# Kernel tuning notes

Measured on AMD Instinct MI355X. Metric: run time of the kernel, lower is better.

## Reference

```python
import jax, jax.numpy as jnp
import numpy as np

N_SRC = 100000
N_DST = 100000
N_EDGES = 640000
D = 128
D_OUT = 128


def setup_inputs() -> dict:
    key = jax.random.key(0)
    k1, k2, k3, k4, k5, k6 = jax.random.split(key, 6)
    h_src = jax.random.normal(k1, (N_SRC, D), dtype=jnp.float32)
    h_dst = jax.random.normal(k2, (N_DST, D), dtype=jnp.float32)
    src_idx = jax.random.randint(k3, (N_EDGES,), 0, N_SRC, dtype=jnp.int32)
    dst_idx = jax.random.randint(k4, (N_EDGES,), 0, N_DST, dtype=jnp.int32)
    W = jax.random.normal(k5, (2 * D, D_OUT), dtype=jnp.float32) * 0.05
    b = jax.random.normal(k6, (D_OUT,), dtype=jnp.float32) * 0.05
    return {"h_src": h_src, "h_dst": h_dst, "src_idx": src_idx,
            "dst_idx": dst_idx, "W": W, "b": b}


def reference(h_src, h_dst, src_idx, dst_idx, W, b):
    # copy_u: gather source features along edges -> [E, D]
    msgs = h_src[src_idx]
    # mean aggregation per destination node (segment mean)
    summed = jax.ops.segment_sum(msgs, dst_idx, num_segments=N_DST)  # [N_dst, D]
    deg = jax.ops.segment_sum(jnp.ones((N_EDGES,), dtype=h_src.dtype),
                              dst_idx, num_segments=N_DST)  # [N_dst]
    h_N = summed / jnp.maximum(deg, 1.0)[:, None]
    # concat self + neighbor mean, then linear projection
    h_total = jnp.concatenate([h_dst, h_N], axis=1)  # [N_dst, 2D]
    return h_total @ W + b
```

## Files before the change

### kernel.cpp

```cpp
#include <hip/hip_runtime.h>

#define D 128
#define N_SRC 100000
#define N_DST 100000
#define N_EDGES 640000

#define SCAN_BLK 1024
#define N_SCAN_BLOCKS ((N_DST + SCAN_BLK - 1) / SCAN_BLK)

#define HIST_BLOCKS ((N_EDGES + 255) / 256)
#define CVT_BLOCKS  ((N_SRC * D / 8) / 256)
#define PACKW_BLOCKS 128

typedef __attribute__((ext_vector_type(8))) short s8v;
typedef __attribute__((ext_vector_type(4))) float f32x4;

__device__ __forceinline__ unsigned short f2bf(float f) {
    unsigned int u = __float_as_uint(f);
    u += 0x7fffu + ((u >> 16) & 1u);
    return (unsigned short)(u >> 16);
}

__device__ __forceinline__ unsigned int pk2(float a, float b) {
    return (unsigned int)f2bf(a) | ((unsigned int)f2bf(b) << 16);
}

__global__ __launch_bounds__(256) void prep(
    const int* __restrict__ dst_idx, int* __restrict__ counts,
    const float* __restrict__ h_src, unsigned int* __restrict__ mir32,
    const float* __restrict__ W, unsigned short* __restrict__ Bp)
{
    const int blk = blockIdx.x;
    const int tid = threadIdx.x;
    if (blk < HIST_BLOCKS) {
        int e = blk * 256 + tid;
        if (e < N_EDGES) atomicAdd(&counts[dst_idx[e]], 1);
    } else if (blk < HIST_BLOCKS + CVT_BLOCKS) {
        int id = (blk - HIST_BLOCKS) * 256 + tid;
        size_t e = (size_t)id * 8;
        const float4* p = (const float4*)(h_src + e);
        float4 x = p[0], y = p[1];
        uint4 o;
        o.x = pk2(x.x, x.y); o.y = pk2(x.z, x.w);
        o.z = pk2(y.x, y.y); o.w = pk2(y.z, y.w);
        *(uint4*)(mir32 + (size_t)(id >> 4) * 64 + (id & 15) * 4) = o;
    } else {
        int id = (blk - HIST_BLOCKS - CVT_BLOCKS) * 256 + tid;
        if (id < 32768) {
            int j = id & 7;
            int l = (id >> 3) & 63;
            int t = (id >> 9) & 7;
            int s = id >> 12;
            int k = s * 32 + (l >> 4) * 8 + j;
            int n = t * 16 + (l & 15);
            Bp[id] = f2bf(W[k * D + n]);
        }
    }
}


__global__ __launch_bounds__(256) void scan_blocks(
    const int* __restrict__ counts, int* __restrict__ row_start,
    int* __restrict__ block_sums)
{
    __shared__ int sh[256];
    const int tid = threadIdx.x;
    const int base = blockIdx.x * SCAN_BLK + tid * 4;
    int v[4];
    int local = 0;
#pragma unroll
    for (int k = 0; k < 4; k++) {
        int idx = base + k;
        v[k] = (idx < N_DST) ? counts[idx] : 0;
        local += v[k];
    }
    sh[tid] = local;
    __syncthreads();
    for (int off = 1; off < 256; off <<= 1) {
        int t = (tid >= off) ? sh[tid - off] : 0;
        __syncthreads();
        sh[tid] += t;
        __syncthreads();
    }
    int run = (tid == 0) ? 0 : sh[tid - 1];
    if (tid == 255) block_sums[blockIdx.x] = sh[255];
#pragma unroll
    for (int k = 0; k < 4; k++) {
        int idx = base + k;
        if (idx < N_DST) row_start[idx] = run;
        run += v[k];
    }
}

__global__ __launch_bounds__(256) void add_offsets(
    int* __restrict__ row_start, const int* __restrict__ block_sums,
    int* __restrict__ cursor)
{
    __shared__ int sh[128];
    const int tid = threadIdx.x;
    if (tid < 128) sh[tid] = (tid < N_SCAN_BLOCKS) ? block_sums[tid] : 0;
    __syncthreads();
    for (int off = 1; off < 128; off <<= 1) {
        int t = (tid < 128 && tid >= off) ? sh[tid - off] : 0;
        __syncthreads();
        if (tid < 128) sh[tid] += t;
        __syncthreads();
    }
    int i = blockIdx.x * 256 + tid;
    if (i < N_DST) {
        int blk = i / SCAN_BLK;
        int off = (blk == 0) ? 0 : sh[blk - 1];
        int v = row_start[i] + off;
        row_start[i] = v;
        cursor[i] = v;
    }
    if (i == 0) row_start[N_DST] = N_EDGES;
}

__global__ __launch_bounds__(256) void scatter_perm(
    const int* __restrict__ src_idx, const int* __restrict__ dst_idx,
    int* __restrict__ cursor, int* __restrict__ edge_src)
{
    int e = blockIdx.x * 256 + threadIdx.x;
    if (e < N_EDGES) {
        int d = dst_idx[e];
        int pos = atomicAdd(&cursor[d], 1);
        edge_src[pos] = src_idx[e];
    }
}

__global__ __launch_bounds__(128, 4) void fused_ag(
    const float* __restrict__ h_dst,
    const unsigned short* __restrict__ mir,
    const int* __restrict__ row_start,
    const int* __restrict__ edge_src,
    const unsigned short* __restrict__ Bp,
    const float* __restrict__ bias,
    float* __restrict__ out)
{
    __shared__ uint4 hN4[512];
    char* hN = (char*)hN4;

    const int tid = threadIdx.x;
    const int wave = tid >> 6;
    const int lane = tid & 63;
    const int quad = lane >> 4;
    const int lr = lane & 15;
    const int rw0 = blockIdx.x * 32 + wave * 16;

#pragma unroll
    for (int i = 0; i < 4; i++) {
        int rl = wave * 16 + i * 4 + quad;
        int row = blockIdx.x * 32 + rl;
        int start = row_start[row];
        int deg = row_start[row + 1] - start;
        float a[8] = {0.f, 0.f, 0.f, 0.f, 0.f, 0.f, 0.f, 0.f};
        for (int base = 0; base < deg; base += 8) {
            int j = base + (lr & 7);
            int myid = edge_src[start + min(j, deg - 1)];
#pragma unroll
            for (int t = 0; t < 8; t++) {
                int s = __shfl(myid, t, 16);
                uint4 u = *(const uint4*)(mir + (size_t)s * 128 + lr * 8);
                float m = ((base + t) < deg) ? 1.f : 0.f;
                a[0] = fmaf(__uint_as_float(u.x << 16), m, a[0]);
                a[1] = fmaf(__uint_as_float(u.x & 0xffff0000u), m, a[1]);
                a[2] = fmaf(__uint_as_float(u.y << 16), m, a[2]);
                a[3] = fmaf(__uint_as_float(u.y & 0xffff0000u), m, a[3]);
                a[4] = fmaf(__uint_as_float(u.z << 16), m, a[4]);
                a[5] = fmaf(__uint_as_float(u.z & 0xffff0000u), m, a[5]);
                a[6] = fmaf(__uint_as_float(u.w << 16), m, a[6]);
                a[7] = fmaf(__uint_as_float(u.w & 0xffff0000u), m, a[7]);
            }
        }
        float inv = 1.0f / fmaxf((float)deg, 1.0f);
        uint4 o;
        o.x = pk2(a[0] * inv, a[1] * inv);
        o.y = pk2(a[2] * inv, a[3] * inv);
        o.z = pk2(a[4] * inv, a[5] * inv);
        o.w = pk2(a[6] * inv, a[7] * inv);
        int ba = (rl * 256 + lr * 16) ^ ((rl & 7) << 4);
        *(uint4*)(hN + ba) = o;
    }

    s8v an[4];
    {
        int rl = wave * 16 + lr;
#pragma unroll
        for (int s = 0; s < 4; s++) {
            int ba = (rl * 256 + s * 64 + quad * 16) ^ ((rl & 7) << 4);
            an[s] = *(const s8v*)(hN + ba);
        }
    }

    const int r0 = rw0 + lr;
    const float* p0 = h_dst + (size_t)r0 * D + quad * 8;
    float4 x0[4], y0[4];
#pragma unroll
    for (int s = 0; s < 4; s++) {
        x0[s] = *(const float4*)(p0 + s * 32);
        y0[s] = *(const float4*)(p0 + s * 32 + 4);
    }
    s8v af0[4];
#pragma unroll
    for (int s = 0; s < 4; s++) {
        unsigned short u0[8];
        u0[0]=f2bf(x0[s].x); u0[1]=f2bf(x0[s].y); u0[2]=f2bf(x0[s].z); u0[3]=f2bf(x0[s].w);
        u0[4]=f2bf(y0[s].x); u0[5]=f2bf(y0[s].y); u0[6]=f2bf(y0[s].z); u0[7]=f2bf(y0[s].w);
        af0[s] = *(s8v*)u0;
    }

    f32x4 acc[8];
#pragma unroll
    for (int t = 0; t < 8; t++) acc[t] = (f32x4){0.f, 0.f, 0.f, 0.f};

#pragma unroll
    for (int s = 0; s < 8; s++) {
        s8v a0 = (s < 4) ? af0[s] : an[s - 4];
#pragma unroll
        for (int t = 0; t < 8; t++) {
            s8v bf = *(const s8v*)(Bp + ((size_t)(s * 8 + t) * 64 + lane) * 8);
            acc[t] = __builtin_amdgcn_mfma_f32_16x16x32_bf16(a0, bf, acc[t], 0, 0, 0);
        }
    }

#pragma unroll
    for (int t = 0; t < 8; t++) {
        float bv = bias[t * 16 + lr];
#pragma unroll
        for (int r = 0; r < 4; r++) {
            int row = rw0 + quad * 4 + r;
            out[(size_t)row * D + t * 16 + lr] = acc[t][r] + bv;
        }
    }
}

extern "C" void kernel_launch(void* const* d_in, const int* in_sizes, int n_in,
                              void* d_out, int out_size, void* d_ws, size_t ws_size,
                              hipStream_t stream) {
    const float* h_src  = (const float*)d_in[0];
    const float* h_dst  = (const float*)d_in[1];
    const int* src_idx  = (const int*)d_in[2];
    const int* dst_idx  = (const int*)d_in[3];
    const float* W      = (const float*)d_in[4];
    const float* b      = (const float*)d_in[5];
    float* out = (float*)d_out;

    unsigned short* Bp = (unsigned short*)d_ws;
    int* ws_i          = (int*)((char*)d_ws + 65536);
    int* row_start     = ws_i;
    int* cursor        = row_start + (N_DST + 1);
    int* counts        = cursor + N_DST;
    int* block_sums    = counts + N_DST;
    int* edge_src      = block_sums + N_SCAN_BLOCKS;

    size_t int_bytes = (size_t)(N_DST + 1 + N_DST + N_DST + N_SCAN_BLOCKS + N_EDGES) * 4;
    size_t mir_off   = (65536 + int_bytes + 255) & ~(size_t)255;
    unsigned short* mir = (unsigned short*)((char*)d_ws + mir_off);

    hipMemsetAsync(counts, 0, (size_t)N_DST * sizeof(int), stream);

    prep<<<HIST_BLOCKS + CVT_BLOCKS + PACKW_BLOCKS, 256, 0, stream>>>(
        dst_idx, counts, h_src, (unsigned int*)mir, W, Bp);
    scan_blocks<<<N_SCAN_BLOCKS, 256, 0, stream>>>(counts, row_start, block_sums);
    add_offsets<<<(N_DST + 255) / 256, 256, 0, stream>>>(row_start, block_sums, cursor);
    scatter_perm<<<(N_EDGES + 255) / 256, 256, 0, stream>>>(src_idx, dst_idx, cursor, edge_src);

    fused_ag<<<N_DST / 32, 128, 0, stream>>>(
        h_dst, mir, row_start, edge_src, Bp, b, out);
}
```

Before: 258.2 us.

## Merge CSR build into one persistent kernel with grid barriers; widen aggregation blocks

Replaces the memset plus prep, scan, offset and scatter launches with a single persistent 1024-block kernel that uses atomic grid barriers between phases, removing several launch gaps and kernel boundaries. The aggregation kernel moves to 256-thread blocks covering 64 rows each. Its inner loop splits full 8-edge groups, which read edge ids directly without shuffles or masking, from a masked tail group. The grid barrier relies on all 1024 blocks being co-resident and could deadlock if they are not. Reading edge ids per lane instead of shuffling adds redundant scalar loads.

```diff
diff --git a/kernel.cpp b/kernel.cpp
--- a/kernel.cpp
+++ b/kernel.cpp
@@ -8,9 +8,8 @@
 #define SCAN_BLK 1024
 #define N_SCAN_BLOCKS ((N_DST + SCAN_BLK - 1) / SCAN_BLK)
 
-#define HIST_BLOCKS ((N_EDGES + 255) / 256)
-#define CVT_BLOCKS  ((N_SRC * D / 8) / 256)
-#define PACKW_BLOCKS 128
+#define CSR_BLOCKS 1024
+#define CSR_THREADS (CSR_BLOCKS * 256)
 
 typedef __attribute__((ext_vector_type(8))) short s8v;
 typedef __attribute__((ext_vector_type(4))) float f32x4;
@@ -25,79 +24,83 @@
     return (unsigned int)f2bf(a) | ((unsigned int)f2bf(b) << 16);
 }
 
-__global__ __launch_bounds__(256) void prep(
-    const int* __restrict__ dst_idx, int* __restrict__ counts,
-    const float* __restrict__ h_src, unsigned int* __restrict__ mir32,
-    const float* __restrict__ W, unsigned short* __restrict__ Bp)
+__device__ __forceinline__ void grid_barrier(int* ctr) {
+    __syncthreads();
+    if (threadIdx.x == 0) {
+        __threadfence();
+        __hip_atomic_fetch_add(ctr, 1, __ATOMIC_RELEASE, __HIP_MEMORY_SCOPE_AGENT);
+        while (__hip_atomic_load(ctr, __ATOMIC_ACQUIRE, __HIP_MEMORY_SCOPE_AGENT)
+               < CSR_BLOCKS) {}
+    }
+    __syncthreads();
+}
+
+__global__ __launch_bounds__(256, 4) void build_csr(
+    const float* __restrict__ h_src,
+    const int* __restrict__ src_idx, const int* __restrict__ dst_idx,
+    const float* __restrict__ W,
+    unsigned int* __restrict__ mir32, unsigned short* __restrict__ Bp,
+    int* __restrict__ counts, int* __restrict__ row_start,
+    int* __restrict__ cursor, int* __restrict__ block_sums,
+    int* __restrict__ edge_src, int* __restrict__ bar)
 {
-    const int blk = blockIdx.x;
+    __shared__ int sh[256];
     const int tid = threadIdx.x;
-    if (blk < HIST_BLOCKS) {
-        int e = blk * 256 + tid;
-        if (e < N_EDGES) atomicAdd(&counts[dst_idx[e]], 1);
-    } else if (blk < HIST_BLOCKS + CVT_BLOCKS) {
-        int id = (blk - HIST_BLOCKS) * 256 + tid;
-        size_t e = (size_t)id * 8;
-        const float4* p = (const float4*)(h_src + e);
+    const int gid = blockIdx.x * 256 + tid;
+
+    for (int i = gid; i < N_DST; i += CSR_THREADS) counts[i] = 0;
+    for (int id = gid; id < N_SRC * 16; id += CSR_THREADS) {
+        const float4* p = (const float4*)(h_src + (size_t)id * 8);
         float4 x = p[0], y = p[1];
         uint4 o;
         o.x = pk2(x.x, x.y); o.y = pk2(x.z, x.w);
         o.z = pk2(y.x, y.y); o.w = pk2(y.z, y.w);
         *(uint4*)(mir32 + (size_t)(id >> 4) * 64 + (id & 15) * 4) = o;
-    } else {
-        int id = (blk - HIST_BLOCKS - CVT_BLOCKS) * 256 + tid;
-        if (id < 32768) {
-            int j = id & 7;
-            int l = (id >> 3) & 63;
-            int t = (id >> 9) & 7;
-            int s = id >> 12;
-            int k = s * 32 + (l >> 4) * 8 + j;
-            int n = t * 16 + (l & 15);
-            Bp[id] = f2bf(W[k * D + n]);
-        }
-    }
-}
-
-
-__global__ __launch_bounds__(256) void scan_blocks(
-    const int* __restrict__ counts, int* __restrict__ row_start,
-    int* __restrict__ block_sums)
-{
-    __shared__ int sh[256];
-    const int tid = threadIdx.x;
-    const int base = blockIdx.x * SCAN_BLK + tid * 4;
-    int v[4];
-    int local = 0;
-#pragma unroll
-    for (int k = 0; k < 4; k++) {
-        int idx = base + k;
-        v[k] = (idx < N_DST) ? counts[idx] : 0;
-        local += v[k];
-    }
-    sh[tid] = local;
-    __syncthreads();
-    for (int off = 1; off < 256; off <<= 1) {
-        int t = (tid >= off) ? sh[tid - off] : 0;
+    }
+    for (int id = gid; id < 32768; id += CSR_THREADS) {
+        int j = id & 7;
+        int l = (id >> 3) & 63;
+        int t = (id >> 9) & 7;
+        int s = id >> 12;
+        int k = s * 32 + (l >> 4) * 8 + j;
+        int n = t * 16 + (l & 15);
+        Bp[id] = f2bf(W[k * D + n]);
+    }
+    grid_barrier(&bar[0]);
+
+    for (int e = gid; e < N_EDGES; e += CSR_THREADS)
+        atomicAdd(&counts[dst_idx[e]], 1);
+    grid_barrier(&bar[1]);
+
+    if (blockIdx.x < N_SCAN_BLOCKS) {
+        const int base = blockIdx.x * SCAN_BLK + tid * 4;
+        int v[4];
+        int local = 0;
+#pragma unroll
+        for (int k = 0; k < 4; k++) {
+            int idx = base + k;
+            v[k] = (idx < N_DST) ? counts[idx] : 0;
+            local += v[k];
+        }
+        sh[tid] = local;
         __syncthreads();
-        sh[tid] += t;
-        __syncthreads();
-    }
-    int run = (tid == 0) ? 0 : sh[tid - 1];
-    if (tid == 255) block_sums[blockIdx.x] = sh[255];
-#pragma unroll
-    for (int k = 0; k < 4; k++) {
-        int idx = base + k;
-        if (idx < N_DST) row_start[idx] = run;
-        run += v[k];
-    }
-}
-
-__global__ __launch_bounds__(256) void add_offsets(
-    int* __restrict__ row_start, const int* __restrict__ block_sums,
-    int* __restrict__ cursor)
-{
-    __shared__ int sh[128];
-    const int tid = threadIdx.x;
+        for (int off = 1; off < 256; off <<= 1) {
+            int t = (tid >= off) ? sh[tid - off] : 0;
+            __syncthreads();
+            sh[tid] += t;
+            __syncthreads();
+        }
+        int run = (tid == 0) ? 0 : sh[tid - 1];
+        if (tid == 255) block_sums[blockIdx.x] = sh[255];
+#pragma unroll
+        for (int k = 0; k < 4; k++) {
+            int idx = base + k;
+            if (idx < N_DST) row_start[idx] = run;
+            run += v[k];
+        }
+    }
+    grid_barrier(&bar[2]);
+
     if (tid < 128) sh[tid] = (tid < N_SCAN_BLOCKS) ? block_sums[tid] : 0;
     __syncthreads();
     for (int off = 1; off < 128; off <<= 1) {
@@ -106,30 +109,24 @@
         if (tid < 128) sh[tid] += t;
         __syncthreads();
     }
-    int i = blockIdx.x * 256 + tid;
-    if (i < N_DST) {
+    for (int i = gid; i < N_DST; i += CSR_THREADS) {
         int blk = i / SCAN_BLK;
         int off = (blk == 0) ? 0 : sh[blk - 1];
         int v = row_start[i] + off;
         row_start[i] = v;
         cursor[i] = v;
     }
-    if (i == 0) row_start[N_DST] = N_EDGES;
-}
-
-__global__ __launch_bounds__(256) void scatter_perm(
-    const int* __restrict__ src_idx, const int* __restrict__ dst_idx,
-    int* __restrict__ cursor, int* __restrict__ edge_src)
-{
-    int e = blockIdx.x * 256 + threadIdx.x;
-    if (e < N_EDGES) {
+    if (gid == 0) row_start[N_DST] = N_EDGES;
+    grid_barrier(&bar[3]);
+
+    for (int e = gid; e < N_EDGES; e += CSR_THREADS) {
         int d = dst_idx[e];
         int pos = atomicAdd(&cursor[d], 1);
         edge_src[pos] = src_idx[e];
     }
 }
 
-__global__ __launch_bounds__(128, 4) void fused_ag(
+__global__ __launch_bounds__(256, 4) void fused_ag(
     const float* __restrict__ h_dst,
     const unsigned short* __restrict__ mir,
     const int* __restrict__ row_start,
@@ -138,7 +135,7 @@
     const float* __restrict__ bias,
     float* __restrict__ out)
 {
-    __shared__ uint4 hN4[512];
+    __shared__ uint4 hN4[1024];
     char* hN = (char*)hN4;
 
     const int tid = threadIdx.x;
@@ -146,23 +143,39 @@
     const int lane = tid & 63;
     const int quad = lane >> 4;
     const int lr = lane & 15;
-    const int rw0 = blockIdx.x * 32 + wave * 16;
+    const int wg = blockIdx.x * 4 + wave;
+    if (wg * 16 >= N_DST) return;
+    const int rw0 = wg * 16;
 
 #pragma unroll
     for (int i = 0; i < 4; i++) {
         int rl = wave * 16 + i * 4 + quad;
-        int row = blockIdx.x * 32 + rl;
+        int row = blockIdx.x * 64 + rl;
         int start = row_start[row];
         int deg = row_start[row + 1] - start;
+        int nfull = deg & ~7;
         float a[8] = {0.f, 0.f, 0.f, 0.f, 0.f, 0.f, 0.f, 0.f};
-        for (int base = 0; base < deg; base += 8) {
-            int j = base + (lr & 7);
-            int myid = edge_src[start + min(j, deg - 1)];
+        for (int base = 0; base < nfull; base += 8) {
 #pragma unroll
             for (int t = 0; t < 8; t++) {
-                int s = __shfl(myid, t, 16);
+                int s = edge_src[start + base + t];
                 uint4 u = *(const uint4*)(mir + (size_t)s * 128 + lr * 8);
-                float m = ((base + t) < deg) ? 1.f : 0.f;
+                a[0] += __uint_as_float(u.x << 16);
+                a[1] += __uint_as_float(u.x & 0xffff0000u);
+                a[2] += __uint_as_float(u.y << 16);
+                a[3] += __uint_as_float(u.y & 0xffff0000u);
+                a[4] += __uint_as_float(u.z << 16);
+                a[5] += __uint_as_float(u.z & 0xffff0000u);
+                a[6] += __uint_as_float(u.w << 16);
+                a[7] += __uint_as_float(u.w & 0xffff0000u);
+            }
+        }
+        if (nfull < deg) {
+#pragma unroll
+            for (int t = 0; t < 8; t++) {
+                int s = edge_src[start + min(nfull + t, deg - 1)];
+                uint4 u = *(const uint4*)(mir + (size_t)s * 128 + lr * 8);
+                float m = ((nfull + t) < deg) ? 1.f : 0.f;
                 a[0] = fmaf(__uint_as_float(u.x << 16), m, a[0]);
                 a[1] = fmaf(__uint_as_float(u.x & 0xffff0000u), m, a[1]);
                 a[2] = fmaf(__uint_as_float(u.y << 16), m, a[2]);
@@ -252,20 +265,21 @@
     int* cursor        = row_start + (N_DST + 1);
     int* counts        = cursor + N_DST;
     int* block_sums    = counts + N_DST;
-    int* edge_src      = block_sums + N_SCAN_BLOCKS;
-
-    size_t int_bytes = (size_t)(N_DST + 1 + N_DST + N_DST + N_SCAN_BLOCKS + N_EDGES) * 4;
+    int* bar           = block_sums + N_SCAN_BLOCKS;
+    int* edge_src      = bar + 8;
+
+    size_t int_bytes = (size_t)(N_DST + 1 + N_DST + N_DST + N_SCAN_BLOCKS + 8
+                                + N_EDGES) * 4;
     size_t mir_off   = (65536 + int_bytes + 255) & ~(size_t)255;
     unsigned short* mir = (unsigned short*)((char*)d_ws + mir_off);
 
-    hipMemsetAsync(counts, 0, (size_t)N_DST * sizeof(int), stream);
-
-    prep<<<HIST_BLOCKS + CVT_BLOCKS + PACKW_BLOCKS, 256, 0, stream>>>(
-        dst_idx, counts, h_src, (unsigned int*)mir, W, Bp);
-    scan_blocks<<<N_SCAN_BLOCKS, 256, 0, stream>>>(counts, row_start, block_sums);
-    add_offsets<<<(N_DST + 255) / 256, 256, 0, stream>>>(row_start, block_sums, cursor);
-    scatter_perm<<<(N_EDGES + 255) / 256, 256, 0, stream>>>(src_idx, dst_idx, cursor, edge_src);
-
-    fused_ag<<<N_DST / 32, 128, 0, stream>>>(
+    hipMemsetAsync(bar, 0, 8 * sizeof(int), stream);
+
+    build_csr<<<CSR_BLOCKS, 256, 0, stream>>>(
+        h_src, src_idx, dst_idx, W,
+        (unsigned int*)mir, Bp,
+        counts, row_start, cursor, block_sums, edge_src, bar);
+
+    fused_ag<<<(N_DST + 63) / 64, 256, 0, stream>>>(
         h_dst, mir, row_start, edge_src, Bp, b, out);
 }
```

After: 725.0 us. 2.81x slower.

## Move bf16 conversion into scatter pass, widen aggregation blocks, unmask full edge chunks

Applied to the files above, without the earlier changes.

The bf16 conversion of h_src and the W packing move out of the histogram kernel and into the scatter kernel, so the histogram atomics run alone and the conversion shares a launch with the scatter. The aggregation kernel goes from 128 to 256 threads per block, handling 64 rows per block, with a guard for waves past the end. Full 8-edge chunks now read edge indices directly and accumulate with plain adds instead of a lane shuffle and a masked FMA. Only the tail chunk keeps the masked path. The cost is a larger shared-memory footprint per block and a slightly different schedule of atomics against conversion traffic.

```diff
diff --git a/kernel.cpp b/kernel.cpp
--- a/kernel.cpp
+++ b/kernel.cpp
@@ -8,7 +8,7 @@
 #define SCAN_BLK 1024
 #define N_SCAN_BLOCKS ((N_DST + SCAN_BLK - 1) / SCAN_BLK)
 
-#define HIST_BLOCKS ((N_EDGES + 255) / 256)
+#define SCAT_BLOCKS ((N_EDGES + 255) / 256)
 #define CVT_BLOCKS  ((N_SRC * D / 8) / 256)
 #define PACKW_BLOCKS 128
 
@@ -25,27 +25,96 @@
     return (unsigned int)f2bf(a) | ((unsigned int)f2bf(b) << 16);
 }
 
-__global__ __launch_bounds__(256) void prep(
-    const int* __restrict__ dst_idx, int* __restrict__ counts,
+__global__ __launch_bounds__(256) void hist_kernel(
+    const int* __restrict__ dst_idx, int* __restrict__ counts)
+{
+    int e = blockIdx.x * 256 + threadIdx.x;
+    if (e < N_EDGES) atomicAdd(&counts[dst_idx[e]], 1);
+}
+
+__global__ __launch_bounds__(256) void scan_blocks(
+    const int* __restrict__ counts, int* __restrict__ row_start,
+    int* __restrict__ block_sums)
+{
+    __shared__ int sh[256];
+    const int tid = threadIdx.x;
+    const int base = blockIdx.x * SCAN_BLK + tid * 4;
+    int v[4];
+    int local = 0;
+#pragma unroll
+    for (int k = 0; k < 4; k++) {
+        int idx = base + k;
+        v[k] = (idx < N_DST) ? counts[idx] : 0;
+        local += v[k];
+    }
+    sh[tid] = local;
+    __syncthreads();
+    for (int off = 1; off < 256; off <<= 1) {
+        int t = (tid >= off) ? sh[tid - off] : 0;
+        __syncthreads();
+        sh[tid] += t;
+        __syncthreads();
+    }
+    int run = (tid == 0) ? 0 : sh[tid - 1];
+    if (tid == 255) block_sums[blockIdx.x] = sh[255];
+#pragma unroll
+    for (int k = 0; k < 4; k++) {
+        int idx = base + k;
+        if (idx < N_DST) row_start[idx] = run;
+        run += v[k];
+    }
+}
+
+__global__ __launch_bounds__(256) void add_offsets(
+    int* __restrict__ row_start, const int* __restrict__ block_sums,
+    int* __restrict__ cursor)
+{
+    __shared__ int sh[128];
+    const int tid = threadIdx.x;
+    if (tid < 128) sh[tid] = (tid < N_SCAN_BLOCKS) ? block_sums[tid] : 0;
+    __syncthreads();
+    for (int off = 1; off < 128; off <<= 1) {
+        int t = (tid < 128 && tid >= off) ? sh[tid - off] : 0;
+        __syncthreads();
+        if (tid < 128) sh[tid] += t;
+        __syncthreads();
+    }
+    int i = blockIdx.x * 256 + tid;
+    if (i < N_DST) {
+        int blk = i / SCAN_BLK;
+        int off = (blk == 0) ? 0 : sh[blk - 1];
+        int v = row_start[i] + off;
+        row_start[i] = v;
+        cursor[i] = v;
+    }
+    if (i == 0) row_start[N_DST] = N_EDGES;
+}
+
+__global__ __launch_bounds__(256) void scatter_cvt(
+    const int* __restrict__ src_idx, const int* __restrict__ dst_idx,
+    int* __restrict__ cursor, int* __restrict__ edge_src,
     const float* __restrict__ h_src, unsigned int* __restrict__ mir32,
     const float* __restrict__ W, unsigned short* __restrict__ Bp)
 {
     const int blk = blockIdx.x;
     const int tid = threadIdx.x;
-    if (blk < HIST_BLOCKS) {
+    if (blk < SCAT_BLOCKS) {
         int e = blk * 256 + tid;
-        if (e < N_EDGES) atomicAdd(&counts[dst_idx[e]], 1);
-    } else if (blk < HIST_BLOCKS + CVT_BLOCKS) {
-        int id = (blk - HIST_BLOCKS) * 256 + tid;
-        size_t e = (size_t)id * 8;
-        const float4* p = (const float4*)(h_src + e);
+        if (e < N_EDGES) {
+            int d = dst_idx[e];
+            int pos = atomicAdd(&cursor[d], 1);
+            edge_src[pos] = src_idx[e];
+        }
+    } else if (blk < SCAT_BLOCKS + CVT_BLOCKS) {
+        int id = (blk - SCAT_BLOCKS) * 256 + tid;
+        const float4* p = (const float4*)(h_src + (size_t)id * 8);
         float4 x = p[0], y = p[1];
         uint4 o;
         o.x = pk2(x.x, x.y); o.y = pk2(x.z, x.w);
         o.z = pk2(y.x, y.y); o.w = pk2(y.z, y.w);
         *(uint4*)(mir32 + (size_t)(id >> 4) * 64 + (id & 15) * 4) = o;
     } else {
-        int id = (blk - HIST_BLOCKS - CVT_BLOCKS) * 256 + tid;
+        int id = (blk - SCAT_BLOCKS - CVT_BLOCKS) * 256 + tid;
         if (id < 32768) {
             int j = id & 7;
             int l = (id >> 3) & 63;
@@ -58,78 +127,7 @@
     }
 }
 
-
-__global__ __launch_bounds__(256) void scan_blocks(
-    const int* __restrict__ counts, int* __restrict__ row_start,
-    int* __restrict__ block_sums)
-{
-    __shared__ int sh[256];
-    const int tid = threadIdx.x;
-    const int base = blockIdx.x * SCAN_BLK + tid * 4;
-    int v[4];
-    int local = 0;
-#pragma unroll
-    for (int k = 0; k < 4; k++) {
-        int idx = base + k;
-        v[k] = (idx < N_DST) ? counts[idx] : 0;
-        local += v[k];
-    }
-    sh[tid] = local;
-    __syncthreads();
-    for (int off = 1; off < 256; off <<= 1) {
-        int t = (tid >= off) ? sh[tid - off] : 0;
-        __syncthreads();
-        sh[tid] += t;
-        __syncthreads();
-    }
-    int run = (tid == 0) ? 0 : sh[tid - 1];
-    if (tid == 255) block_sums[blockIdx.x] = sh[255];
-#pragma unroll
-    for (int k = 0; k < 4; k++) {
-        int idx = base + k;
-        if (idx < N_DST) row_start[idx] = run;
-        run += v[k];
-    }
-}
-
-__global__ __launch_bounds__(256) void add_offsets(
-    int* __restrict__ row_start, const int* __restrict__ block_sums,
-    int* __restrict__ cursor)
-{
-    __shared__ int sh[128];
-    const int tid = threadIdx.x;
-    if (tid < 128) sh[tid] = (tid < N_SCAN_BLOCKS) ? block_sums[tid] : 0;
-    __syncthreads();
-    for (int off = 1; off < 128; off <<= 1) {
-        int t = (tid < 128 && tid >= off) ? sh[tid - off] : 0;
-        __syncthreads();
-        if (tid < 128) sh[tid] += t;
-        __syncthreads();
-    }
-    int i = blockIdx.x * 256 + tid;
-    if (i < N_DST) {
-        int blk = i / SCAN_BLK;
-        int off = (blk == 0) ? 0 : sh[blk - 1];
-        int v = row_start[i] + off;
-        row_start[i] = v;
-        cursor[i] = v;
-    }
-    if (i == 0) row_start[N_DST] = N_EDGES;
-}
-
-__global__ __launch_bounds__(256) void scatter_perm(
-    const int* __restrict__ src_idx, const int* __restrict__ dst_idx,
-    int* __restrict__ cursor, int* __restrict__ edge_src)
-{
-    int e = blockIdx.x * 256 + threadIdx.x;
-    if (e < N_EDGES) {
-        int d = dst_idx[e];
-        int pos = atomicAdd(&cursor[d], 1);
-        edge_src[pos] = src_idx[e];
-    }
-}
-
-__global__ __launch_bounds__(128, 4) void fused_ag(
+__global__ __launch_bounds__(256, 4) void fused_ag(
     const float* __restrict__ h_dst,
     const unsigned short* __restrict__ mir,
     const int* __restrict__ row_start,
@@ -138,7 +136,7 @@
     const float* __restrict__ bias,
     float* __restrict__ out)
 {
-    __shared__ uint4 hN4[512];
+    __shared__ uint4 hN4[1024];
     char* hN = (char*)hN4;
 
     const int tid = threadIdx.x;
@@ -146,23 +144,39 @@
     const int lane = tid & 63;
     const int quad = lane >> 4;
     const int lr = lane & 15;
-    const int rw0 = blockIdx.x * 32 + wave * 16;
+    const int wg = blockIdx.x * 4 + wave;
+    if (wg * 16 >= N_DST) return;
+    const int rw0 = wg * 16;
 
 #pragma unroll
     for (int i = 0; i < 4; i++) {
         int rl = wave * 16 + i * 4 + quad;
-        int row = blockIdx.x * 32 + rl;
+        int row = blockIdx.x * 64 + rl;
         int start = row_start[row];
         int deg = row_start[row + 1] - start;
+        int nfull = deg & ~7;
         float a[8] = {0.f, 0.f, 0.f, 0.f, 0.f, 0.f, 0.f, 0.f};
-        for (int base = 0; base < deg; base += 8) {
-            int j = base + (lr & 7);
-            int myid = edge_src[start + min(j, deg - 1)];
+        for (int base = 0; base < nfull; base += 8) {
 #pragma unroll
             for (int t = 0; t < 8; t++) {
-                int s = __shfl(myid, t, 16);
+                int s = edge_src[start + base + t];
                 uint4 u = *(const uint4*)(mir + (size_t)s * 128 + lr * 8);
-                float m = ((base + t) < deg) ? 1.f : 0.f;
+                a[0] += __uint_as_float(u.x << 16);
+                a[1] += __uint_as_float(u.x & 0xffff0000u);
+                a[2] += __uint_as_float(u.y << 16);
+                a[3] += __uint_as_float(u.y & 0xffff0000u);
+                a[4] += __uint_as_float(u.z << 16);
+                a[5] += __uint_as_float(u.z & 0xffff0000u);
+                a[6] += __uint_as_float(u.w << 16);
+                a[7] += __uint_as_float(u.w & 0xffff0000u);
+            }
+        }
+        if (nfull < deg) {
+#pragma unroll
+            for (int t = 0; t < 8; t++) {
+                int s = edge_src[start + min(nfull + t, deg - 1)];
+                uint4 u = *(const uint4*)(mir + (size_t)s * 128 + lr * 8);
+                float m = ((nfull + t) < deg) ? 1.f : 0.f;
                 a[0] = fmaf(__uint_as_float(u.x << 16), m, a[0]);
                 a[1] = fmaf(__uint_as_float(u.x & 0xffff0000u), m, a[1]);
                 a[2] = fmaf(__uint_as_float(u.y << 16), m, a[2]);
@@ -254,18 +268,21 @@
     int* block_sums    = counts + N_DST;
     int* edge_src      = block_sums + N_SCAN_BLOCKS;
 
-    size_t int_bytes = (size_t)(N_DST + 1 + N_DST + N_DST + N_SCAN_BLOCKS + N_EDGES) * 4;
+    size_t int_bytes = (size_t)(N_DST + 1 + N_DST + N_DST + N_SCAN_BLOCKS
+                                + N_EDGES) * 4;
     size_t mir_off   = (65536 + int_bytes + 255) & ~(size_t)255;
     unsigned short* mir = (unsigned short*)((char*)d_ws + mir_off);
 
     hipMemsetAsync(counts, 0, (size_t)N_DST * sizeof(int), stream);
 
-    prep<<<HIST_BLOCKS + CVT_BLOCKS + PACKW_BLOCKS, 256, 0, stream>>>(
-        dst_idx, counts, h_src, (unsigned int*)mir, W, Bp);
+    hist_kernel<<<(N_EDGES + 255) / 256, 256, 0, stream>>>(dst_idx, counts);
     scan_blocks<<<N_SCAN_BLOCKS, 256, 0, stream>>>(counts, row_start, block_sums);
     add_offsets<<<(N_DST + 255) / 256, 256, 0, stream>>>(row_start, block_sums, cursor);
-    scatter_perm<<<(N_EDGES + 255) / 256, 256, 0, stream>>>(src_idx, dst_idx, cursor, edge_src);
-
-    fused_ag<<<N_DST / 32, 128, 0, stream>>>(
+
+    scatter_cvt<<<SCAT_BLOCKS + CVT_BLOCKS + PACKW_BLOCKS, 256, 0, stream>>>(
+        src_idx, dst_idx, cursor, edge_src,
+        h_src, (unsigned int*)mir, W, Bp);
+
+    fused_ag<<<(N_DST + 63) / 64, 256, 0, stream>>>(
         h_dst, mir, row_start, edge_src, Bp, b, out);
 }
```

Result: no change. 257.7 us (-0.2%).
